# Performance work log

Hardware: AMD Instinct MI355X
Metric: run time of the kernel (lower is better)

Reference implementation:

```python
import jax, jax.numpy as jnp
import numpy as np

B, P0, P1, P2 = 8, 20000, 5000, 1250
M, W = 10, 9
C0, C1, C2 = 3, 64, 128
LATENT = 256


def _pad(x):
    # append one zero 'ghost' point row (pad index == in_point_num)
    return jnp.concatenate([x, jnp.zeros_like(x[:, :1])], axis=1)


def _full_conv(x, nb, w_weights, weights, bias, c_out):
    # x: [B, in_pn, Cin], nb: [P, M] (values in [0, in_pn], in_pn == pad)
    in_pn = x.shape[1]
    c_in = x.shape[-1]
    xp = _pad(x)                                   # [B, in_pn+1, Cin]
    mask = (nb != in_pn).astype(x.dtype)           # [P, M]
    nbh = xp[:, nb]                                # [B, P, M, Cin]
    w2 = w_weights * mask[..., None]               # [P, M, W]
    wpm = jnp.einsum('pmw,wc->pmc', w2, weights)   # [P, M, Cout*Cin]
    wpm = wpm.reshape(nb.shape[0], M, c_out, c_in)
    return jnp.einsum('pmoi,bpmi->bpo', wpm, nbh) + bias


def _pool(x, nb, p_nb):
    in_pn = x.shape[1]
    xp = _pad(x)
    mask = (nb != in_pn).astype(x.dtype)           # [P, M]
    nbh = xp[:, nb]                                # [B, P, M, C]
    p = jnp.abs(p_nb) * mask
    p = p / (p.sum(1, keepdims=True) + 1e-8)
    return jnp.einsum('pm,bpmc->bpc', p, nbh)


def setup_inputs() -> dict:
    key = jax.random.key(0)
    ks = jax.random.split(key, 16)
    avg_nb = float(M)
    inp = {
        'x': jax.random.normal(ks[0], (B, P0, C0), dtype=jnp.float32),
        'nb0': jax.random.randint(ks[1], (P0, M), 0, P0 + 1),
        'nb1': jax.random.randint(ks[2], (P1, M), 0, P0 + 1),
        'nb2': jax.random.randint(ks[3], (P1, M), 0, P1 + 1),
        'nb3': jax.random.randint(ks[4], (P2, M), 0, P1 + 1),
        # full conv layer 0: 3 -> 64 @ 20000 points
        'weights0': jax.random.normal(ks[5], (W, C1 * C0), dtype=jnp.float32),
        'bias0': jnp.zeros((C1,), dtype=jnp.float32),
        'w_weights0': jax.random.normal(ks[6], (P0, M, W), dtype=jnp.float32) / (avg_nb * W),
        # pool layer 1: 20000 -> 5000, channels unchanged
        'p_neighbors1': jax.random.normal(ks[7], (P1, M), dtype=jnp.float32) / avg_nb,
        # full conv layer 2: 64 -> 128 @ 5000 points
        'weights2': jax.random.normal(ks[8], (W, C2 * C1), dtype=jnp.float32),
        'bias2': jnp.zeros((C2,), dtype=jnp.float32),
        'w_weights2': jax.random.normal(ks[9], (P1, M, W), dtype=jnp.float32) / (avg_nb * W),
        # pool layer 3: 5000 -> 1250, channels unchanged
        'p_neighbors3': jax.random.normal(ks[10], (P2, M), dtype=jnp.float32) / avg_nb,
        # latent heads
        'W_miu': jax.random.normal(ks[11], (LATENT, P2 * C2), dtype=jnp.float32) * 0.01,
        'b_miu': jnp.zeros((LATENT,), dtype=jnp.float32),
        'W_sigma': jax.random.normal(ks[12], (LATENT, P2 * C2), dtype=jnp.float32) * 0.01,
        'b_sigma': jnp.zeros((LATENT,), dtype=jnp.float32),
    }
    return inp


def reference(x, nb0, nb1, nb2, nb3, weights0, bias0, w_weights0, p_neighbors1,
              weights2, bias2, w_weights2, p_neighbors3, W_miu, b_miu, W_sigma, b_sigma):
    h = jax.nn.elu(_full_conv(x, nb0, w_weights0, weights0, bias0, C1))   # [B, P0, 64]
    h = jax.nn.elu(_pool(h, nb1, p_neighbors1))                           # [B, P1, 64]
    h = jax.nn.elu(_full_conv(h, nb2, w_weights2, weights2, bias2, C2))   # [B, P1, 128]
    h = jax.nn.elu(_pool(h, nb3, p_neighbors3))                           # [B, P2, 128]
    f = h.reshape(h.shape[0], -1)                                         # [B, P2*C2]
    miu = f @ W_miu.T + b_miu
    sigma = f @ W_sigma.T + b_sigma
    return jnp.concatenate([miu, sigma], axis=-1)                         # [B, 2*LATENT]
```

## Files before the change

### kernel.cpp

```cpp
#include <hip/hip_runtime.h>

#define Bx 8
#define P0 20000
#define P1 5000
#define P2 1250
#define Mn 10
#define Wn 9
#define C0 3
#define C1 64
#define C2 128
#define KF 160000

typedef float f32x4 __attribute__((ext_vector_type(4)));
typedef short bf16x8 __attribute__((ext_vector_type(8)));

__device__ __forceinline__ float elu_f(float x){ return x > 0.f ? x : expm1f(x); }

__device__ __forceinline__ unsigned short f2bf(float x){
    union { float f; unsigned u; } v; v.f = x;
    unsigned r = v.u + 0x7fffu + ((v.u >> 16) & 1u);
    return (unsigned short)(r >> 16);
}
__device__ __forceinline__ float bf2f(unsigned short h){
    union { unsigned u; float f; } v; v.u = ((unsigned)h) << 16; return v.f;
}

__global__ __launch_bounds__(256) void k_wpack(const float* __restrict__ w2,
                                               unsigned short* __restrict__ wT){
    int idx = blockIdx.x * 256 + threadIdx.x;
    int j  = idx & 7;
    int l  = (idx >> 3) & 63;
    int g  = idx >> 9;
    int ot = g & 7, s = g >> 3;
    int o  = ot * 16 + (l & 15);
    int k  = s * 32 + (l >> 4) * 8 + j;
    int w  = k >> 6, i = k & 63;
    wT[idx] = f2bf(w2[w * (C2 * C1) + o * C1 + i]);
}

__global__ __launch_bounds__(256) void k_conv0(const float* __restrict__ x,
                                               const int* __restrict__ nb0,
                                               const float* __restrict__ weights0,
                                               const float* __restrict__ bias0,
                                               const float* __restrict__ w_weights0,
                                               float* __restrict__ h0){
    __shared__ int   s_nb[Mn];
    __shared__ float s_w2[Mn * Wn];
    __shared__ float s_xh[Bx * Mn * C0];
    __shared__ float s_g[Bx * 27];
    __shared__ float s_wt[27 * 64];
    int p = blockIdx.x, t = threadIdx.x;

    if (t < Mn) s_nb[t] = nb0[p * Mn + t];
    __syncthreads();
    if (t < Mn * Wn){
        int m = t / Wn;
        s_w2[t] = w_weights0[p * Mn * Wn + t] * (s_nb[m] != P0 ? 1.f : 0.f);
    }
    if (t < Bx * Mn * C0){
        int b = t / (Mn * C0), r = t % (Mn * C0), m = r / C0, i = r % C0;
        int idx = s_nb[m];
        s_xh[t] = (idx < P0) ? x[((size_t)b * P0 + idx) * C0 + i] : 0.f;
    }
    for (int e = t; e < 27 * 64; e += 256){
        int k = e >> 6, o = e & 63, w = k / 3, i = k - w * 3;
        s_wt[e] = weights0[w * (C1 * C0) + o * C0 + i];
    }
    __syncthreads();
    if (t < Bx * 27){
        int b = t / 27, k = t % 27, w = k / 3, i = k - w * 3;
        float a = 0.f;
        #pragma unroll
        for (int m = 0; m < Mn; ++m) a += s_w2[m * Wn + w] * s_xh[b * (Mn * C0) + m * C0 + i];
        s_g[t] = a;
    }
    __syncthreads();
    int b = t >> 5, o = (t & 31) * 2;
    float ax = bias0[o], ay = bias0[o + 1];
    #pragma unroll
    for (int k = 0; k < 27; ++k){
        float gv = s_g[b * 27 + k];
        ax += gv * s_wt[k * 64 + o];
        ay += gv * s_wt[k * 64 + o + 1];
    }
    float2 r; r.x = elu_f(ax); r.y = elu_f(ay);
    *(float2*)&h0[((size_t)b * P0 + p) * C1 + o] = r;
}

__global__ __launch_bounds__(256) void k_pool1(const float* __restrict__ hin,
                                               const int* __restrict__ nb,
                                               const float* __restrict__ pnb,
                                               float* __restrict__ hout){
    __shared__ int   s_nb[Mn];
    __shared__ float s_pa[Mn];
    __shared__ float s_pw[Mn];
    int p = blockIdx.x, t = threadIdx.x;
    if (t < Mn){ s_nb[t] = nb[p * Mn + t]; s_pa[t] = pnb[p * Mn + t]; }
    __syncthreads();
    if (t < Mn){
        float denom = 1e-8f;
        for (int m = 0; m < Mn; ++m) denom += fabsf(s_pa[m]) * (s_nb[m] != P0 ? 1.f : 0.f);
        s_pw[t] = fabsf(s_pa[t]) * (s_nb[t] != P0 ? 1.f : 0.f) / denom;
    }
    __syncthreads();
    int b = t >> 5, c = (t & 31) * 2;
    float ax = 0.f, ay = 0.f;
    #pragma unroll
    for (int m = 0; m < Mn; ++m){
        int idx = s_nb[m];
        if (idx < P0){
            float wv = s_pw[m];
            const float2 v = *(const float2*)&hin[((size_t)b * P0 + idx) * C1 + c];
            ax += wv * v.x; ay += wv * v.y;
        }
    }
    float2 r; r.x = elu_f(ax); r.y = elu_f(ay);
    *(float2*)&hout[((size_t)b * P1 + p) * C1 + c] = r;
}

__global__ __launch_bounds__(256) void k_conv2(const float* __restrict__ h1,
                                               const int* __restrict__ nb2,
                                               const float* __restrict__ w_weights2,
                                               const float* __restrict__ bias2,
                                               const unsigned short* __restrict__ wT,
                                               float* __restrict__ h2){
    __shared__ int   s_nb[2][Mn];
    __shared__ float s_w2[2][Mn * Wn];
    __shared__ __align__(16) unsigned short s_gh[16 * 584];
    __shared__ __align__(16) unsigned short s_gl[16 * 584];
    int t = threadIdx.x;
    int p1b = blockIdx.x * 2;

    if (t < 2 * Mn){ int q = t / Mn, m = t % Mn; s_nb[q][m] = nb2[(p1b + q) * Mn + m]; }
    __syncthreads();
    if (t < 2 * Mn * Wn){
        int q = t / (Mn * Wn), r = t % (Mn * Wn), m = r / Wn;
        s_w2[q][r] = w_weights2[(size_t)(p1b + q) * Mn * Wn + r] * (s_nb[q][m] != P1 ? 1.f : 0.f);
    }
    __syncthreads();
    {
        int q = t >> 7, b = (t >> 4) & 7, ig = t & 15;
        float gx[Wn], gy[Wn], gz[Wn], gw[Wn];
        #pragma unroll
        for (int w = 0; w < Wn; ++w){ gx[w] = 0.f; gy[w] = 0.f; gz[w] = 0.f; gw[w] = 0.f; }
        #pragma unroll
        for (int m = 0; m < Mn; ++m){
            int idx = s_nb[q][m];
            if (idx < P1){
                const float4 v = *(const float4*)&h1[((size_t)b * P1 + idx) * C1 + ig * 4];
                #pragma unroll
                for (int w = 0; w < Wn; ++w){
                    float ww = s_w2[q][m * Wn + w];
                    gx[w] += ww * v.x; gy[w] += ww * v.y; gz[w] += ww * v.z; gw[w] += ww * v.w;
                }
            }
        }
        int r = q * 8 + b;
        #pragma unroll
        for (int w = 0; w < Wn; ++w){
            int base = r * 584 + w * 64 + ig * 4;
            ushort4 hh, ll;
            hh.x = f2bf(gx[w]); ll.x = f2bf(gx[w] - bf2f(hh.x));
            hh.y = f2bf(gy[w]); ll.y = f2bf(gy[w] - bf2f(hh.y));
            hh.z = f2bf(gz[w]); ll.z = f2bf(gz[w] - bf2f(hh.z));
            hh.w = f2bf(gw[w]); ll.w = f2bf(gw[w] - bf2f(hh.w));
            *(ushort4*)&s_gh[base] = hh;
            *(ushort4*)&s_gl[base] = ll;
        }
    }
    __syncthreads();
    {
        int wave = t >> 6, lane = t & 63;
        int n16 = lane & 15, quad = lane >> 4;
        f32x4 acc0 = {0.f, 0.f, 0.f, 0.f};
        f32x4 acc1 = {0.f, 0.f, 0.f, 0.f};
        const unsigned short* pAh = s_gh + n16 * 584 + quad * 8;
        const unsigned short* pAl = s_gl + n16 * 584 + quad * 8;
        int ot0 = wave * 2, ot1 = ot0 + 1;
        const unsigned short* pB0 = wT + ot0 * 512 + lane * 8;
        const unsigned short* pB1 = wT + ot1 * 512 + lane * 8;
        #pragma unroll
        for (int s = 0; s < 18; ++s){
            bf16x8 ah = *(const bf16x8*)(pAh + s * 32);
            bf16x8 al = *(const bf16x8*)(pAl + s * 32);
            bf16x8 b0 = *(const bf16x8*)(pB0 + s * 4096);
            bf16x8 b1 = *(const bf16x8*)(pB1 + s * 4096);
            acc0 = __builtin_amdgcn_mfma_f32_16x16x32_bf16(al, b0, acc0, 0, 0, 0);
            acc0 = __builtin_amdgcn_mfma_f32_16x16x32_bf16(ah, b0, acc0, 0, 0, 0);
            acc1 = __builtin_amdgcn_mfma_f32_16x16x32_bf16(al, b1, acc1, 0, 0, 0);
            acc1 = __builtin_amdgcn_mfma_f32_16x16x32_bf16(ah, b1, acc1, 0, 0, 0);
        }
        int o0 = ot0 * 16 + n16, o1 = ot1 * 16 + n16;
        float bb0 = bias2[o0], bb1 = bias2[o1];
        #pragma unroll
        for (int reg = 0; reg < 4; ++reg){
            int r = quad * 4 + reg;
            int q = r >> 3, b = r & 7;
            size_t row = ((size_t)b * P1 + (p1b + q)) * C2;
            h2[row + o0] = elu_f(acc0[reg] + bb0);
            h2[row + o1] = elu_f(acc1[reg] + bb1);
        }
    }
}

__global__ __launch_bounds__(256) void k_pool3(const float* __restrict__ h2,
                                               const int* __restrict__ nb3,
                                               const float* __restrict__ pnb,
                                               float* __restrict__ f){
    __shared__ int   s_nb[Mn];
    __shared__ float s_pa[Mn];
    __shared__ float s_pw[Mn];
    int p = blockIdx.x, t = threadIdx.x;
    if (t < Mn){ s_nb[t] = nb3[p * Mn + t]; s_pa[t] = pnb[p * Mn + t]; }
    __syncthreads();
    if (t < Mn){
        float denom = 1e-8f;
        for (int m = 0; m < Mn; ++m) denom += fabsf(s_pa[m]) * (s_nb[m] != P1 ? 1.f : 0.f);
        s_pw[t] = fabsf(s_pa[t]) * (s_nb[t] != P1 ? 1.f : 0.f) / denom;
    }
    __syncthreads();
    int b = t >> 5, c = (t & 31) * 4;
    float ax = 0.f, ay = 0.f, az = 0.f, aw = 0.f;
    #pragma unroll
    for (int m = 0; m < Mn; ++m){
        int idx = s_nb[m];
        if (idx < P1){
            float wv = s_pw[m];
            const float4 v = *(const float4*)&h2[((size_t)b * P1 + idx) * C2 + c];
            ax += wv * v.x; ay += wv * v.y; az += wv * v.z; aw += wv * v.w;
        }
    }
    float4 r; r.x = elu_f(ax); r.y = elu_f(ay); r.z = elu_f(az); r.w = elu_f(aw);
    *(float4*)&f[(size_t)b * KF + (size_t)p * C2 + c] = r;
}

__global__ __launch_bounds__(256) void k_init_out(const float* __restrict__ b_miu,
                                                  const float* __restrict__ b_sigma,
                                                  float* __restrict__ out){
    int tid = blockIdx.x * 256 + threadIdx.x;
    if (tid < Bx * 512){
        int l = tid & 511;
        out[tid] = (l < 256) ? b_miu[l] : b_sigma[l - 256];
    }
}

__global__ __launch_bounds__(256) void k_final(const float* __restrict__ f,
                                               const float* __restrict__ Wm,
                                               const float* __restrict__ Ws,
                                               float* __restrict__ out){
    int t = threadIdx.x;
    int lg = blockIdx.x & 63, kc = blockIdx.x >> 6;
    int l0 = lg * 8;
    const float* Wrow[8];
    #pragma unroll
    for (int i = 0; i < 8; ++i){
        int li = l0 + i;
        Wrow[i] = (li < 256) ? (Wm + (size_t)li * KF) : (Ws + (size_t)(li - 256) * KF);
    }
    float acc[64];
    #pragma unroll
    for (int a = 0; a < 64; ++a) acc[a] = 0.f;

    int e0 = kc * 1250, e1 = e0 + 1250;
    for (int e = e0 + t; e < e1; e += 256){
        float4 fv[8];
        #pragma unroll
        for (int b = 0; b < 8; ++b) fv[b] = *(const float4*)&f[(size_t)b * KF + (size_t)e * 4];
        #pragma unroll
        for (int i = 0; i < 8; ++i){
            const float4 wv = *(const float4*)&Wrow[i][(size_t)e * 4];
            #pragma unroll
            for (int b = 0; b < 8; ++b)
                acc[i * 8 + b] += wv.x * fv[b].x + wv.y * fv[b].y + wv.z * fv[b].z + wv.w * fv[b].w;
        }
    }
    __shared__ float s_red[4][64];
    int wave = t >> 6, lane = t & 63;
    #pragma unroll
    for (int a = 0; a < 64; ++a){
        float v = acc[a];
        v += __shfl_down(v, 32); v += __shfl_down(v, 16); v += __shfl_down(v, 8);
        v += __shfl_down(v, 4);  v += __shfl_down(v, 2);  v += __shfl_down(v, 1);
        if (lane == 0) s_red[wave][a] = v;
    }
    __syncthreads();
    if (t < 64){
        float v = s_red[0][t] + s_red[1][t] + s_red[2][t] + s_red[3][t];
        int i = t >> 3, b = t & 7;
        atomicAdd(&out[b * 512 + l0 + i], v);
    }
}

extern "C" void kernel_launch(void* const* d_in, const int* in_sizes, int n_in,
                              void* d_out, int out_size, void* d_ws, size_t ws_size,
                              hipStream_t stream){
    const float* x            = (const float*)d_in[0];
    const int*   nb0          = (const int*)d_in[1];
    const int*   nb1          = (const int*)d_in[2];
    const int*   nb2          = (const int*)d_in[3];
    const int*   nb3          = (const int*)d_in[4];
    const float* weights0     = (const float*)d_in[5];
    const float* bias0        = (const float*)d_in[6];
    const float* w_weights0   = (const float*)d_in[7];
    const float* p_neighbors1 = (const float*)d_in[8];
    const float* weights2     = (const float*)d_in[9];
    const float* bias2        = (const float*)d_in[10];
    const float* w_weights2   = (const float*)d_in[11];
    const float* p_neighbors3 = (const float*)d_in[12];
    const float* W_miu        = (const float*)d_in[13];
    const float* b_miu        = (const float*)d_in[14];
    const float* W_sigma      = (const float*)d_in[15];
    const float* b_sigma      = (const float*)d_in[16];
    float* out = (float*)d_out;

    float* wsf = (float*)d_ws;
    float* h0 = wsf;
    float* h1 = wsf + 10240000;
    float* h2 = wsf;
    float* f  = wsf + 5120000;
    unsigned short* wT = (unsigned short*)(wsf + 12800000);

    k_wpack<<<288, 256, 0, stream>>>(weights2, wT);
    k_conv0<<<P0, 256, 0, stream>>>(x, nb0, weights0, bias0, w_weights0, h0);
    k_pool1<<<P1, 256, 0, stream>>>(h0, nb1, p_neighbors1, h1);
    k_conv2<<<P1 / 2, 256, 0, stream>>>(h1, nb2, w_weights2, bias2, wT, h2);
    k_pool3<<<P2, 256, 0, stream>>>(h2, nb3, p_neighbors3, f);
    k_init_out<<<16, 256, 0, stream>>>(b_miu, b_sigma, out);
    k_final<<<2048, 256, 0, stream>>>(f, W_miu, W_sigma, out);
}
```

Baseline: 541.9 us.

## Restructure final GEMV to stage feature chunks in LDS with wave-per-row

The latent-head matmul kernel now loads a 1280-wide chunk of all 8 batch feature rows into shared memory once per block, and each of 8 waves computes one output row against that chunk. Per-wave shuffle reductions feed atomicAdds directly, which removes the 64-register accumulator array and the cross-wave shared reduction. The grid grows to 8000 blocks of 512 threads. This cuts register pressure and raises occupancy and parallelism for a bandwidth-bound weight stream, at the cost of many more atomics and a 40KB LDS footprint per block.

```diff
diff --git a/kernel.cpp b/kernel.cpp
--- a/kernel.cpp
+++ b/kernel.cpp
@@ -10,6 +10,7 @@
 #define C1 64
 #define C2 128
 #define KF 160000
+#define KCH 1280
 
 typedef float f32x4 __attribute__((ext_vector_type(4)));
 typedef short bf16x8 __attribute__((ext_vector_type(8)));
@@ -244,50 +245,50 @@
     }
 }
 
-__global__ __launch_bounds__(256) void k_final(const float* __restrict__ f,
+__global__ __launch_bounds__(512) void k_final(const float* __restrict__ f,
                                                const float* __restrict__ Wm,
                                                const float* __restrict__ Ws,
                                                float* __restrict__ out){
+    __shared__ __align__(16) float s_f[Bx * KCH];
     int t = threadIdx.x;
-    int lg = blockIdx.x & 63, kc = blockIdx.x >> 6;
-    int l0 = lg * 8;
-    const float* Wrow[8];
-    #pragma unroll
-    for (int i = 0; i < 8; ++i){
-        int li = l0 + i;
-        Wrow[i] = (li < 256) ? (Wm + (size_t)li * KF) : (Ws + (size_t)(li - 256) * KF);
-    }
-    float acc[64];
-    #pragma unroll
-    for (int a = 0; a < 64; ++a) acc[a] = 0.f;
-
-    int e0 = kc * 1250, e1 = e0 + 1250;
-    for (int e = e0 + t; e < e1; e += 256){
-        float4 fv[8];
-        #pragma unroll
-        for (int b = 0; b < 8; ++b) fv[b] = *(const float4*)&f[(size_t)b * KF + (size_t)e * 4];
-        #pragma unroll
-        for (int i = 0; i < 8; ++i){
-            const float4 wv = *(const float4*)&Wrow[i][(size_t)e * 4];
-            #pragma unroll
-            for (int b = 0; b < 8; ++b)
-                acc[i * 8 + b] += wv.x * fv[b].x + wv.y * fv[b].y + wv.z * fv[b].z + wv.w * fv[b].w;
-        }
-    }
-    __shared__ float s_red[4][64];
+    int bx = blockIdx.x;
+    int lg = bx / 125, kc = bx % 125;
+    int k0 = kc * KCH;
+
+    #pragma unroll
+    for (int it = 0; it < 5; ++it){
+        int i = it * 512 + t;
+        int b = i / 320; int e = i - b * 320;
+        *(float4*)&s_f[b * KCH + e * 4] =
+            *(const float4*)&f[(size_t)b * KF + (size_t)(k0 + e * 4)];
+    }
+    __syncthreads();
+
     int wave = t >> 6, lane = t & 63;
-    #pragma unroll
-    for (int a = 0; a < 64; ++a){
-        float v = acc[a];
+    int l = lg * 8 + wave;
+    const float* Wrow = ((l < 256) ? (Wm + (size_t)l * KF)
+                                   : (Ws + (size_t)(l - 256) * KF)) + k0;
+    float acc[8];
+    #pragma unroll
+    for (int b = 0; b < 8; ++b) acc[b] = 0.f;
+
+    #pragma unroll
+    for (int it = 0; it < 5; ++it){
+        int e = it * 64 + lane;
+        const float4 wv = *(const float4*)&Wrow[e * 4];
+        #pragma unroll
+        for (int b = 0; b < 8; ++b){
+            const float4 fv = *(const float4*)&s_f[b * KCH + e * 4];
+            acc[b] += wv.x * fv.x + wv.y * fv.y + wv.z * fv.z + wv.w * fv.w;
+        }
+    }
+
+    #pragma unroll
+    for (int b = 0; b < 8; ++b){
+        float v = acc[b];
         v += __shfl_down(v, 32); v += __shfl_down(v, 16); v += __shfl_down(v, 8);
         v += __shfl_down(v, 4);  v += __shfl_down(v, 2);  v += __shfl_down(v, 1);
-        if (lane == 0) s_red[wave][a] = v;
-    }
-    __syncthreads();
-    if (t < 64){
-        float v = s_red[0][t] + s_red[1][t] + s_red[2][t] + s_red[3][t];
-        int i = t >> 3, b = t & 7;
-        atomicAdd(&out[b * 512 + l0 + i], v);
+        if (lane == 0) atomicAdd(&out[b * 512 + l], v);
     }
 }
 
@@ -326,5 +327,5 @@
     k_conv2<<<P1 / 2, 256, 0, stream>>>(h1, nb2, w_weights2, bias2, wT, h2);
     k_pool3<<<P2, 256, 0, stream>>>(h2, nb3, p_neighbors3, f);
     k_init_out<<<16, 256, 0, stream>>>(b_miu, b_sigma, out);
-    k_final<<<2048, 256, 0, stream>>>(f, W_miu, W_sigma, out);
-}
+    k_final<<<64 * 125, 512, 0, stream>>>(f, W_miu, W_sigma, out);
+}
```

Result: slower. 763.5 us (+40.9%).
